# Kernel optimization log

Measured on AMD Instinct MI355X. Metric: run time of the kernel, lower is better.

Reference implementation:

```python
import jax, jax.numpy as jnp
import numpy as np

NUM_HEADS = 8
D_MODEL = 256
D_K = 256
SEQ = 32
FFT_HEAD = 3  # heads >= 3 operate in the FFT domain and are IFFT'd after
NEG = jnp.float32(1e10)


def _fft_t(x):
    # x: (..., 32, 256) real. Interleaved real/imag pairs -> complex 2D FFT over (4,2).
    lead = x.shape[:-2]
    xr = x.reshape(lead + (16, 32, 4, 2, 2))
    xc = jax.lax.complex(xr[..., 0], xr[..., 1])      # (..., 16, 32, 4, 2)
    y = jnp.fft.fft2(xc)                              # over last two axes
    out = jnp.concatenate([jnp.real(y), jnp.imag(y)], axis=-1)  # (...,16,32,4,4)
    return out.reshape(lead + (SEQ, D_MODEL))


def _ifft_t(x):
    lead = x.shape[:-2]
    xr = x.reshape(lead + (16, 32, 4, 2, 2))
    xc = jax.lax.complex(xr[..., 0], xr[..., 1])
    y = jnp.fft.ifft2(xc)
    out = jnp.concatenate([jnp.real(y), jnp.imag(y)], axis=-1)
    return out.reshape(lead + (SEQ, D_MODEL))


def _atrous_mask():
    i = jnp.arange(SEQ)[:, None]
    j = jnp.arange(SEQ)[None, :]
    return (jnp.abs(i - j) % 2 == 0).astype(jnp.float32)  # (32, 32)


def _attn_group(x, Wq_g, Wk_g, Wv_g, mask):
    # x: (B, S, D); W*_g: (H, D, K); mask: (S, S)
    Q = jnp.einsum('bsd,hdk->bhsk', x, Wq_g)
    K = jnp.einsum('bsd,hdk->bhsk', x, Wk_g)
    V = jnp.einsum('bsd,hdk->bhsk', x, Wv_g)
    scores = jnp.einsum('bhsk,bhtk->bhst', Q, K) / jnp.sqrt(jnp.float32(D_K))
    scores = scores * mask - NEG * (1.0 - mask)
    A = jax.nn.softmax(scores, axis=-1)
    return jnp.einsum('bhst,bhtk->bhsk', A, V)  # (B, H, S, K)


def setup_inputs() -> dict:
    key = jax.random.key(0)
    k0, k1, k2, k3 = jax.random.split(key, 4)
    B = 4096
    glorot = float(np.sqrt(2.0 / (D_MODEL + D_K)))
    return {
        'inputs': jax.random.normal(k0, (B, 1, SEQ, D_MODEL), dtype=jnp.float32),
        'Wq': jax.random.normal(k1, (NUM_HEADS, D_MODEL, D_K), dtype=jnp.float32) * glorot,
        'Wk': jax.random.normal(k2, (NUM_HEADS, D_MODEL, D_K), dtype=jnp.float32) * glorot,
        'Wv': jax.random.normal(k3, (NUM_HEADS, D_MODEL, D_K), dtype=jnp.float32) * glorot,
    }


def reference(inputs, Wq, Wk, Wv):
    # inputs: (B, 1, 32, 256)
    x = inputs[:, 0]                                  # (B, 32, 256)
    mask = _atrous_mask()
    # Heads 0..2: plain domain
    out_lo = _attn_group(x, Wq[:FFT_HEAD], Wk[:FFT_HEAD], Wv[:FFT_HEAD], mask)
    # Heads 3..: FFT domain, outputs IFFT'd per head
    xf = _fft_t(x)
    out_hi = _attn_group(xf, Wq[FFT_HEAD:], Wk[FFT_HEAD:], Wv[FFT_HEAD:], mask)
    out_hi = _ifft_t(out_hi)
    total = out_lo.sum(axis=1) + out_hi.sum(axis=1)   # (B, 32, 256)
    return (total / NUM_HEADS)[:, None]               # (B, 1, 32, 256)
```

## Files before the change

### kernel.cpp

```cpp
#include <hip/hip_runtime.h>

typedef _Float16 f16;
typedef _Float16 f16x4 __attribute__((ext_vector_type(4)));
typedef _Float16 f16x8 __attribute__((ext_vector_type(8)));
typedef float    f32x4 __attribute__((ext_vector_type(4)));
typedef unsigned int u32;

#define MFMA_F16(a,b,c) __builtin_amdgcn_mfma_f32_16x16x32_f16((a),(b),(c),0,0,0)

__device__ __forceinline__ u32 pkf16(float a, float b) {
  return __builtin_bit_cast(u32, __builtin_amdgcn_cvt_pkrtz(a, b));
}
union F8U4 { u32 d[4]; f16x8 v; };

__device__ __forceinline__ f16x8 comb(f16x4 a, f16x4 b) {
  f16x8 r;
  #pragma unroll
  for (int i = 0; i < 4; ++i) { r[i] = a[i]; r[4 + i] = b[i]; }
  return r;
}

__device__ __forceinline__ float T_val(int rr, int cc) {
  int p = rr >> 2, f = rr & 3;
  int c = cc >> 2, d = (cc >> 1) & 1, e = cc & 1;
  int q = f & 1;
  int m = (p * c + 2 * q * d) & 3;
  float cs = (m == 0) ? 1.f : (m == 2) ? -1.f : 0.f;
  float sn = (m == 1) ? 1.f : (m == 3) ? -1.f : 0.f;
  if (f < 2) return (e == 0) ? cs : sn;
  return (e == 0) ? -sn : cs;
}
__device__ __forceinline__ float U_val(int rr, int cc) {
  int p = rr >> 2, f = rr & 3;
  int c = cc >> 2, d = (cc >> 1) & 1, e = cc & 1;
  int q = f & 1;
  int m = (p * c + 2 * q * d) & 3;
  float cs = (m == 0) ? 1.f : (m == 2) ? -1.f : 0.f;
  float sn = (m == 1) ? 1.f : (m == 3) ? -1.f : 0.f;
  float v;
  if (f < 2) v = (e == 0) ? cs : -sn;
  else       v = (e == 0) ? sn : cs;
  return v * 0.125f;
}

__global__ void prep_qk(const float* __restrict__ Wq, const float* __restrict__ Wk,
                        float* __restrict__ WqE, float* __restrict__ WkE) {
  int b = blockIdx.x;
  int isK = b >> 11;
  int h = (b >> 8) & 7;
  int dd = b & 255;
  const float* W = isK ? Wk : Wq;
  float* E = isK ? WkE : WqE;
  int k = threadIdx.x;
  size_t base = (size_t)h * 65536;
  float v;
  if (h < 3) {
    v = W[base + (size_t)dd * 256 + k];
  } else {
    int g = dd >> 4, i = dd & 15;
    float s = 0.f;
    for (int ip = 0; ip < 16; ++ip) {
      float t = T_val(ip, i);
      if (t != 0.f) s += t * W[base + (size_t)(g * 16 + ip) * 256 + k];
    }
    v = s;
  }
  E[base + (size_t)dd * 256 + k] = v;
}

__global__ void prep_m(const float* __restrict__ WqE, const float* __restrict__ WkE,
                       f16* __restrict__ Mt) {
  __shared__ float Aq[32][33];
  __shared__ float Bk[32][33];
  int h = blockIdx.x >> 6;
  int dpt = (blockIdx.x >> 3) & 7;
  int dt = blockIdx.x & 7;
  int tid = threadIdx.x;
  int drow = tid & 31;
  int dprow4 = (tid >> 5) * 4;
  float acc0 = 0.f, acc1 = 0.f, acc2 = 0.f, acc3 = 0.f;
  int r = tid >> 3;
  int c0 = (tid & 7) * 4;
  for (int kt = 0; kt < 8; ++kt) {
    for (int jj = 0; jj < 4; ++jj) {
      Aq[r][c0 + jj] = WqE[(size_t)h * 65536 + (size_t)(dt * 32 + r) * 256 + kt * 32 + c0 + jj];
      Bk[r][c0 + jj] = WkE[(size_t)h * 65536 + (size_t)(dpt * 32 + r) * 256 + kt * 32 + c0 + jj];
    }
    __syncthreads();
    #pragma unroll
    for (int k = 0; k < 32; ++k) {
      float a = Aq[drow][k];
      acc0 += a * Bk[dprow4 + 0][k];
      acc1 += a * Bk[dprow4 + 1][k];
      acc2 += a * Bk[dprow4 + 2][k];
      acc3 += a * Bk[dprow4 + 3][k];
    }
    __syncthreads();
  }
  int d_ = dt * 32 + drow;
  size_t ob = (size_t)h * 65536 + (size_t)(dpt * 32 + dprow4) * 256 + d_;
  Mt[ob + 0 * 256] = (f16)(acc0 * 0.0625f);
  Mt[ob + 1 * 256] = (f16)(acc1 * 0.0625f);
  Mt[ob + 2 * 256] = (f16)(acc2 * 0.0625f);
  Mt[ob + 3 * 256] = (f16)(acc3 * 0.0625f);
}

__global__ void prep_v(const float* __restrict__ Wv, f16* __restrict__ Wvt) {
  __shared__ float Ts[16][16];
  __shared__ float Us[16][16];
  int h = blockIdx.x >> 8;
  int kp = blockIdx.x & 255;
  int tid = threadIdx.x;
  Ts[tid >> 4][tid & 15] = T_val(tid >> 4, tid & 15);
  Us[tid >> 4][tid & 15] = U_val(tid >> 4, tid & 15);
  __syncthreads();
  int d = tid;
  int g = d >> 4, i = d & 15;
  int gp = kp >> 4, fp = kp & 15;
  float s = 0.f;
  if (h < 3) {
    s = Wv[(size_t)h * 65536 + (size_t)d * 256 + kp];
  } else {
    for (int ip = 0; ip < 16; ++ip) {
      float tv = Ts[ip][i];
      if (tv != 0.f) {
        float inner = 0.f;
        for (int jj = 0; jj < 16; ++jj) {
          float uv = Us[fp][jj];
          if (uv != 0.f)
            inner += uv * Wv[(size_t)h * 65536 + (size_t)(g * 16 + ip) * 256 + gp * 16 + jj];
        }
        s += tv * inner;
      }
    }
  }
  Wvt[(size_t)h * 65536 + (size_t)kp * 256 + d] = (f16)(s * 0.125f);
}

__global__ void repack16(const f16* __restrict__ Mt, const f16* __restrict__ Wvt,
                         f16* __restrict__ MtF, f16* __restrict__ WvF) {
  int bid = blockIdx.x;
  int which = bid >> 10;
  int h = (bid >> 7) & 7;
  int t16 = (bid >> 3) & 15;
  int kt = bid & 7;
  int l = threadIdx.x;
  const f16* src = which ? Wvt : Mt;
  f16* dst = which ? WvF : MtF;
  size_t sb = (size_t)h * 65536 + (size_t)(t16 * 16 + (l & 15)) * 256 + kt * 32 + (l >> 4) * 8;
  size_t db = ((size_t)((h * 16 + t16) * 8 + kt) * 64 + l) * 8;
  *(f16x8*)(dst + db) = *(const f16x8*)(src + sb);
}

__global__ __launch_bounds__(512, 2) void mha_main(
    const float* __restrict__ xg_all,
    const f16* __restrict__ MtF,
    const f16* __restrict__ WvF,
    float* __restrict__ outG)
{
  extern __shared__ char smem[];
  f16* Xs  = (f16*)smem;
  f16* Y   = (f16*)(smem + 65536);
  f16* Aat = (f16*)(smem + 131072);

  const int tid = threadIdx.x;
  const int w   = tid >> 6;
  const int l   = tid & 63;
  const int l15 = l & 15;
  const int l4  = l >> 4;

  const float* xg = xg_all + (size_t)blockIdx.x * 32768;
  #pragma unroll 4
  for (int i = 0; i < 16; ++i) {
    int f4 = i * 512 + tid;
    int row = f4 >> 6;
    int col = (f4 & 63) << 2;
    f32x4 v = *(const f32x4*)(xg + (size_t)f4 * 4);
    f16x4 hv;
    hv[0] = (f16)v[0]; hv[1] = (f16)v[1]; hv[2] = (f16)v[2]; hv[3] = (f16)v[3];
    *(f16x4*)(Xs + row * 256 + (col ^ ((row & 7) << 3))) = hv;
  }
  __syncthreads();

  const int dq = w >> 1, sh = w & 1;
  const int bp = w >> 2, kq = w & 3;
  const int bq = w >> 1, mt = w & 1;

  f32x4 O[2][2][4];
  #pragma unroll
  for (int b = 0; b < 2; ++b)
    #pragma unroll
    for (int sm = 0; sm < 2; ++sm)
      #pragma unroll
      for (int n = 0; n < 4; ++n)
        O[b][sm][n] = (f32x4){0.f, 0.f, 0.f, 0.f};

  for (int h = 0; h < 8; ++h) {
    {
      f32x4 C[4][4];
      #pragma unroll
      for (int a = 0; a < 4; ++a)
        #pragma unroll
        for (int n = 0; n < 4; ++n) C[a][n] = (f32x4){0.f, 0.f, 0.f, 0.f};
      #pragma unroll 2
      for (int kt = 0; kt < 8; ++kt) {
        f16x8 A[4], B[4];
        #pragma unroll
        for (int a = 0; a < 4; ++a)
          A[a] = *(const f16x8*)(MtF + ((size_t)((h * 16 + dq * 4 + a) * 8 + kt) * 64 + l) * 8);
        #pragma unroll
        for (int n = 0; n < 4; ++n) {
          int srow = sh * 64 + n * 16 + l15;
          B[n] = *(const f16x8*)(Xs + srow * 256 + ((kt * 32 + l4 * 8) ^ ((srow & 7) << 3)));
        }
        #pragma unroll
        for (int a = 0; a < 4; ++a)
          #pragma unroll
          for (int n = 0; n < 4; ++n)
            C[a][n] = MFMA_F16(A[a], B[n], C[a][n]);
      }
      #pragma unroll
      for (int a = 0; a < 4; ++a)
        #pragma unroll
        for (int n = 0; n < 4; ++n) {
          int srow = sh * 64 + n * 16 + l15;
          int dcol = dq * 64 + a * 16 + l4 * 4;
          f16x4 hv;
          hv[0] = (f16)C[a][n][0]; hv[1] = (f16)C[a][n][1];
          hv[2] = (f16)C[a][n][2]; hv[3] = (f16)C[a][n][3];
          *(f16x4*)(Y + srow * 256 + (dcol ^ ((srow & 7) << 3))) = hv;
        }
    }
    u32 Vh[2][2][4][2];
    {
      f32x4 VC[2][2][4];
      #pragma unroll
      for (int b = 0; b < 2; ++b)
        #pragma unroll
        for (int tau = 0; tau < 2; ++tau)
          #pragma unroll
          for (int n = 0; n < 4; ++n) VC[b][tau][n] = (f32x4){0.f, 0.f, 0.f, 0.f};
      #pragma unroll 2
      for (int kt = 0; kt < 8; ++kt) {
        f16x8 Bw[4], Ax[2][2];
        #pragma unroll
        for (int n = 0; n < 4; ++n)
          Bw[n] = *(const f16x8*)(WvF + ((size_t)((h * 16 + kq * 4 + n) * 8 + kt) * 64 + l) * 8);
        #pragma unroll
        for (int b = 0; b < 2; ++b)
          #pragma unroll
          for (int tau = 0; tau < 2; ++tau) {
            int xrow = (bp * 2 + b) * 32 + tau * 16 + l15;
            Ax[b][tau] = *(const f16x8*)(Xs + xrow * 256 + ((kt * 32 + l4 * 8) ^ ((xrow & 7) << 3)));
          }
        #pragma unroll
        for (int b = 0; b < 2; ++b)
          #pragma unroll
          for (int tau = 0; tau < 2; ++tau)
            #pragma unroll
            for (int n = 0; n < 4; ++n)
              VC[b][tau][n] = MFMA_F16(Ax[b][tau], Bw[n], VC[b][tau][n]);
      }
      #pragma unroll
      for (int b = 0; b < 2; ++b)
        #pragma unroll
        for (int tau = 0; tau < 2; ++tau)
          #pragma unroll
          for (int n = 0; n < 4; ++n) {
            Vh[b][tau][n][0] = pkf16(VC[b][tau][n][0], VC[b][tau][n][1]);
            Vh[b][tau][n][1] = pkf16(VC[b][tau][n][2], VC[b][tau][n][3]);
          }
    }
    __syncthreads();

    {
      f32x4 S0 = (f32x4){0.f, 0.f, 0.f, 0.f};
      f32x4 S1 = (f32x4){0.f, 0.f, 0.f, 0.f};
      int yrow = bq * 32 + mt * 16 + l15;
      int x0 = bq * 32 + l15;
      int x1 = bq * 32 + 16 + l15;
      #pragma unroll
      for (int kt = 0; kt < 8; ++kt) {
        int ks = kt * 32 + l4 * 8;
        f16x8 ay = *(const f16x8*)(Y + yrow * 256 + (ks ^ ((yrow & 7) << 3)));
        f16x8 b0 = *(const f16x8*)(Xs + x0 * 256 + (ks ^ ((x0 & 7) << 3)));
        f16x8 b1 = *(const f16x8*)(Xs + x1 * 256 + (ks ^ ((x1 & 7) << 3)));
        S0 = MFMA_F16(ay, b0, S0);
        S1 = MFMA_F16(ay, b1, S1);
      }
      #pragma unroll
      for (int r = 0; r < 4; ++r) {
        bool valid = ((l & 1) == (r & 1));
        float v0 = valid ? S0[r] : -1e30f;
        float v1 = valid ? S1[r] : -1e30f;
        float mx = fmaxf(v0, v1);
        mx = fmaxf(mx, __shfl_xor(mx, 1));
        mx = fmaxf(mx, __shfl_xor(mx, 2));
        mx = fmaxf(mx, __shfl_xor(mx, 4));
        mx = fmaxf(mx, __shfl_xor(mx, 8));
        float e0 = valid ? __expf(v0 - mx) : 0.f;
        float e1 = valid ? __expf(v1 - mx) : 0.f;
        float sm = e0 + e1;
        sm += __shfl_xor(sm, 1);
        sm += __shfl_xor(sm, 2);
        sm += __shfl_xor(sm, 4);
        sm += __shfl_xor(sm, 8);
        float inv = 1.f / sm;
        int s = mt * 16 + l4 * 4 + r;
        Aat[(bq * 32 + s) * 40 + l15] = (f16)(e0 * inv);
        Aat[(bq * 32 + s) * 40 + 16 + l15] = (f16)(e1 * inv);
      }
    }
    __syncthreads();

    #pragma unroll
    for (int b = 0; b < 2; ++b) {
      #pragma unroll
      for (int sm = 0; sm < 2; ++sm) {
        int arow = ((bp * 2 + b) * 32 + sm * 16 + l15) * 40 + l4 * 4;
        f16x8 bf = comb(*(const f16x4*)(Aat + arow),
                        *(const f16x4*)(Aat + arow + 16));
        #pragma unroll
        for (int n = 0; n < 4; ++n) {
          F8U4 av;
          av.d[0] = Vh[b][0][n][0];
          av.d[1] = Vh[b][0][n][1];
          av.d[2] = Vh[b][1][n][0];
          av.d[3] = Vh[b][1][n][1];
          O[b][sm][n] = MFMA_F16(av.v, bf, O[b][sm][n]);
        }
      }
    }
  }

  #pragma unroll
  for (int b = 0; b < 2; ++b) {
    float* ob = outG + ((size_t)blockIdx.x * 4 + bp * 2 + b) * 8192;
    #pragma unroll
    for (int sm = 0; sm < 2; ++sm) {
      int s = sm * 16 + l15;
      #pragma unroll
      for (int n = 0; n < 4; ++n) {
        int kp = kq * 64 + n * 16 + l4 * 4;
        *(f32x4*)(ob + s * 256 + kp) = O[b][sm][n];
      }
    }
  }
}

extern "C" void kernel_launch(void* const* d_in, const int* in_sizes, int n_in,
                              void* d_out, int out_size, void* d_ws, size_t ws_size,
                              hipStream_t stream) {
  const float* x  = (const float*)d_in[0];
  const float* Wq = (const float*)d_in[1];
  const float* Wk = (const float*)d_in[2];
  const float* Wv = (const float*)d_in[3];
  float* out = (float*)d_out;
  char* ws = (char*)d_ws;
  float* WqE = (float*)ws;
  float* WkE = (float*)(ws + 2097152);
  f16*   Mt  = (f16*)(ws + 4194304);
  f16*   Wvt = (f16*)(ws + 5242880);
  f16*   MtF = (f16*)ws;
  f16*   WvF = (f16*)(ws + 2097152);

  prep_qk<<<4096, 256, 0, stream>>>(Wq, Wk, WqE, WkE);
  prep_m<<<512, 256, 0, stream>>>(WqE, WkE, Mt);
  prep_v<<<2048, 256, 0, stream>>>(Wv, Wvt);
  repack16<<<2048, 64, 0, stream>>>(Mt, Wvt, MtF, WvF);
  mha_main<<<1024, 512, 141312, stream>>>(x, MtF, WvF, out);
}
```

Measured before the change: 430.6 us.

## Double block to 1024 threads and halve per-wave tiles in attention kernel

```diff
diff --git a/kernel.cpp b/kernel.cpp
--- a/kernel.cpp
+++ b/kernel.cpp
@@ -152,7 +152,7 @@
   *(f16x8*)(dst + db) = *(const f16x8*)(src + sb);
 }
 
-__global__ __launch_bounds__(512, 2) void mha_main(
+__global__ __launch_bounds__(1024, 4) void mha_main(
     const float* __restrict__ xg_all,
     const f16* __restrict__ MtF,
     const f16* __restrict__ WvF,
@@ -171,8 +171,8 @@
 
   const float* xg = xg_all + (size_t)blockIdx.x * 32768;
   #pragma unroll 4
-  for (int i = 0; i < 16; ++i) {
-    int f4 = i * 512 + tid;
+  for (int i = 0; i < 8; ++i) {
+    int f4 = i * 1024 + tid;
     int row = f4 >> 6;
     int col = (f4 & 63) << 2;
     f32x4 v = *(const f32x4*)(xg + (size_t)f4 * 4);
@@ -182,48 +182,46 @@
   }
   __syncthreads();
 
-  const int dq = w >> 1, sh = w & 1;
-  const int bp = w >> 2, kq = w & 3;
-  const int bq = w >> 1, mt = w & 1;
-
-  f32x4 O[2][2][4];
+  const int dq = w >> 2, sh = w & 3;
+  const int vb = w >> 2, kq = w & 3;
+  const int bq = w >> 2, mt = (w >> 1) & 1, rh = w & 1;
+
+  f32x4 O[2][4];
   #pragma unroll
-  for (int b = 0; b < 2; ++b)
+  for (int sm = 0; sm < 2; ++sm)
     #pragma unroll
-    for (int sm = 0; sm < 2; ++sm)
-      #pragma unroll
-      for (int n = 0; n < 4; ++n)
-        O[b][sm][n] = (f32x4){0.f, 0.f, 0.f, 0.f};
+    for (int n = 0; n < 4; ++n)
+      O[sm][n] = (f32x4){0.f, 0.f, 0.f, 0.f};
 
   for (int h = 0; h < 8; ++h) {
     {
-      f32x4 C[4][4];
+      f32x4 C[4][2];
       #pragma unroll
       for (int a = 0; a < 4; ++a)
         #pragma unroll
-        for (int n = 0; n < 4; ++n) C[a][n] = (f32x4){0.f, 0.f, 0.f, 0.f};
+        for (int n = 0; n < 2; ++n) C[a][n] = (f32x4){0.f, 0.f, 0.f, 0.f};
       #pragma unroll 2
       for (int kt = 0; kt < 8; ++kt) {
-        f16x8 A[4], B[4];
+        f16x8 A[4], B[2];
         #pragma unroll
         for (int a = 0; a < 4; ++a)
           A[a] = *(const f16x8*)(MtF + ((size_t)((h * 16 + dq * 4 + a) * 8 + kt) * 64 + l) * 8);
         #pragma unroll
-        for (int n = 0; n < 4; ++n) {
-          int srow = sh * 64 + n * 16 + l15;
+        for (int n = 0; n < 2; ++n) {
+          int srow = sh * 32 + n * 16 + l15;
           B[n] = *(const f16x8*)(Xs + srow * 256 + ((kt * 32 + l4 * 8) ^ ((srow & 7) << 3)));
         }
         #pragma unroll
         for (int a = 0; a < 4; ++a)
           #pragma unroll
-          for (int n = 0; n < 4; ++n)
+          for (int n = 0; n < 2; ++n)
             C[a][n] = MFMA_F16(A[a], B[n], C[a][n]);
       }
       #pragma unroll
       for (int a = 0; a < 4; ++a)
         #pragma unroll
-        for (int n = 0; n < 4; ++n) {
-          int srow = sh * 64 + n * 16 + l15;
+        for (int n = 0; n < 2; ++n) {
+          int srow = sh * 32 + n * 16 + l15;
           int dcol = dq * 64 + a * 16 + l4 * 4;
           f16x4 hv;
           hv[0] = (f16)C[a][n][0]; hv[1] = (f16)C[a][n][1];
@@ -231,45 +229,37 @@
           *(f16x4*)(Y + srow * 256 + (dcol ^ ((srow & 7) << 3))) = hv;
         }
     }
-    u32 Vh[2][2][4][2];
+    u32 Vh[2][4][2];
     {
-      f32x4 VC[2][2][4];
-      #pragma unroll
-      for (int b = 0; b < 2; ++b)
+      f32x4 VC[2][4];
+      #pragma unroll
+      for (int tau = 0; tau < 2; ++tau)
+        #pragma unroll
+        for (int n = 0; n < 4; ++n) VC[tau][n] = (f32x4){0.f, 0.f, 0.f, 0.f};
+      #pragma unroll 2
+      for (int kt = 0; kt < 8; ++kt) {
+        f16x8 Bw[4], Ax[2];
+        #pragma unroll
+        for (int n = 0; n < 4; ++n)
+          Bw[n] = *(const f16x8*)(WvF + ((size_t)((h * 16 + kq * 4 + n) * 8 + kt) * 64 + l) * 8);
+        #pragma unroll
+        for (int tau = 0; tau < 2; ++tau) {
+          int xrow = vb * 32 + tau * 16 + l15;
+          Ax[tau] = *(const f16x8*)(Xs + xrow * 256 + ((kt * 32 + l4 * 8) ^ ((xrow & 7) << 3)));
+        }
         #pragma unroll
         for (int tau = 0; tau < 2; ++tau)
           #pragma unroll
-          for (int n = 0; n < 4; ++n) VC[b][tau][n] = (f32x4){0.f, 0.f, 0.f, 0.f};
-      #pragma unroll 2
-      for (int kt = 0; kt < 8; ++kt) {
-        f16x8 Bw[4], Ax[2][2];
-        #pragma unroll
-        for (int n = 0; n < 4; ++n)
-          Bw[n] = *(const f16x8*)(WvF + ((size_t)((h * 16 + kq * 4 + n) * 8 + kt) * 64 + l) * 8);
-        #pragma unroll
-        for (int b = 0; b < 2; ++b)
-          #pragma unroll
-          for (int tau = 0; tau < 2; ++tau) {
-            int xrow = (bp * 2 + b) * 32 + tau * 16 + l15;
-            Ax[b][tau] = *(const f16x8*)(Xs + xrow * 256 + ((kt * 32 + l4 * 8) ^ ((xrow & 7) << 3)));
-          }
-        #pragma unroll
-        for (int b = 0; b < 2; ++b)
-          #pragma unroll
-          for (int tau = 0; tau < 2; ++tau)
-            #pragma unroll
-            for (int n = 0; n < 4; ++n)
-              VC[b][tau][n] = MFMA_F16(Ax[b][tau], Bw[n], VC[b][tau][n]);
-      }
-      #pragma unroll
-      for (int b = 0; b < 2; ++b)
-        #pragma unroll
-        for (int tau = 0; tau < 2; ++tau)
-          #pragma unroll
-          for (int n = 0; n < 4; ++n) {
-            Vh[b][tau][n][0] = pkf16(VC[b][tau][n][0], VC[b][tau][n][1]);
-            Vh[b][tau][n][1] = pkf16(VC[b][tau][n][2], VC[b][tau][n][3]);
-          }
+          for (int n = 0; n < 4; ++n)
+            VC[tau][n] = MFMA_F16(Ax[tau], Bw[n], VC[tau][n]);
+      }
+      #pragma unroll
+      for (int tau = 0; tau < 2; ++tau)
+        #pragma unroll
+        for (int n = 0; n < 4; ++n) {
+          Vh[tau][n][0] = pkf16(VC[tau][n][0], VC[tau][n][1]);
+          Vh[tau][n][1] = pkf16(VC[tau][n][2], VC[tau][n][3]);
+        }
     }
     __syncthreads();
 
@@ -289,7 +279,8 @@
         S1 = MFMA_F16(ay, b1, S1);
       }
       #pragma unroll
-      for (int r = 0; r < 4; ++r) {
+      for (int rr = 0; rr < 2; ++rr) {
+        int r = rh * 2 + rr;
         bool valid = ((l & 1) == (r & 1));
         float v0 = valid ? S0[r] : -1e30f;
         float v1 = valid ? S1[r] : -1e30f;
@@ -314,35 +305,31 @@
     __syncthreads();
 
     #pragma unroll
-    for (int b = 0; b < 2; ++b) {
-      #pragma unroll
-      for (int sm = 0; sm < 2; ++sm) {
-        int arow = ((bp * 2 + b) * 32 + sm * 16 + l15) * 40 + l4 * 4;
-        f16x8 bf = comb(*(const f16x4*)(Aat + arow),
-                        *(const f16x4*)(Aat + arow + 16));
-        #pragma unroll
-        for (int n = 0; n < 4; ++n) {
-          F8U4 av;
-          av.d[0] = Vh[b][0][n][0];
-          av.d[1] = Vh[b][0][n][1];
-          av.d[2] = Vh[b][1][n][0];
-          av.d[3] = Vh[b][1][n][1];
-          O[b][sm][n] = MFMA_F16(av.v, bf, O[b][sm][n]);
-        }
-      }
-    }
-  }
-
-  #pragma unroll
-  for (int b = 0; b < 2; ++b) {
-    float* ob = outG + ((size_t)blockIdx.x * 4 + bp * 2 + b) * 8192;
+    for (int sm = 0; sm < 2; ++sm) {
+      int arow = (vb * 32 + sm * 16 + l15) * 40 + l4 * 4;
+      f16x8 bf = comb(*(const f16x4*)(Aat + arow),
+                      *(const f16x4*)(Aat + arow + 16));
+      #pragma unroll
+      for (int n = 0; n < 4; ++n) {
+        F8U4 av;
+        av.d[0] = Vh[0][n][0];
+        av.d[1] = Vh[0][n][1];
+        av.d[2] = Vh[1][n][0];
+        av.d[3] = Vh[1][n][1];
+        O[sm][n] = MFMA_F16(av.v, bf, O[sm][n]);
+      }
+    }
+  }
+
+  {
+    float* ob = outG + ((size_t)blockIdx.x * 4 + vb) * 8192;
     #pragma unroll
     for (int sm = 0; sm < 2; ++sm) {
       int s = sm * 16 + l15;
       #pragma unroll
       for (int n = 0; n < 4; ++n) {
         int kp = kq * 64 + n * 16 + l4 * 4;
-        *(f32x4*)(ob + s * 256 + kp) = O[b][sm][n];
+        *(f32x4*)(ob + s * 256 + kp) = O[sm][n];
       }
     }
   }
@@ -368,5 +355,5 @@
   prep_m<<<512, 256, 0, stream>>>(WqE, WkE, Mt);
   prep_v<<<2048, 256, 0, stream>>>(Wv, Wvt);
   repack16<<<2048, 64, 0, stream>>>(Mt, Wvt, MtF, WvF);
-  mha_main<<<1024, 512, 141312, stream>>>(x, MtF, WvF, out);
-}
+  mha_main<<<1024, 1024, 141312, stream>>>(x, MtF, WvF, out);
+}
```

New measurement: 583.9 us. +35.6%, slower.
